# Performance work log

Measured on AMD Instinct MI355X. Metric: run time of the kernel, lower is better.

Reference implementation:

```python
import jax, jax.numpy as jnp
import numpy as np

B, H, S, DK, DV = 2, 16, 2048, 128, 128


def setup_inputs() -> dict:
    key = jax.random.key(0)
    kq, kk, kv = jax.random.split(key, 3)
    query = jax.random.normal(kq, (B, H, S, DK), dtype=jnp.float32)
    k_ = jax.random.normal(kk, (B, H, S, DK), dtype=jnp.float32)
    value = jax.random.normal(kv, (B, H, S, DV), dtype=jnp.float32)
    # causal mask: True = masked out (upper triangle above diagonal)
    causal = ~jnp.tril(jnp.ones((S, S), dtype=bool))
    mask = jnp.broadcast_to(causal[None, None, :, :], (B, 1, S, S))
    return {"query": query, "key": k_, "value": value, "mask": mask}


def reference(query, key, value, mask):
    d_k = query.shape[-1]
    # scores: (B, H, Sq, Sk)
    scores = jnp.einsum("bhqd,bhkd->bhqk", query, key) / jnp.sqrt(jnp.float32(d_k))
    scores = jnp.where(mask, -jnp.inf, scores)
    attention_weights = jax.nn.softmax(scores, axis=-1)
    # dropout p=0.0 (eval) -> identity
    output = jnp.einsum("bhqk,bhkv->bhqv", attention_weights, value)
    return (output, attention_weights)
```

## Files before the change

### kernel.cpp

```cpp
#include <hip/hip_runtime.h>
#include <hip/hip_bf16.h>


typedef __attribute__((ext_vector_type(4))) float  f32x4;
typedef __attribute__((ext_vector_type(8))) short  short8;
typedef __attribute__((ext_vector_type(4))) short  short4v;

#define S_LEN 2048
#define DKK   128
#define QBLK  128
#define KBLK  64
#define NBH   32
#define NW    8

__device__ __forceinline__ short f2bf(float f) {
    return __builtin_bit_cast(short, __float2bfloat16(f));
}

__device__ __forceinline__ void g2l16(const void* g, void* l) {
    __builtin_amdgcn_global_load_lds(
        (const __attribute__((address_space(1))) unsigned int*)g,
        (__attribute__((address_space(3))) unsigned int*)l, 16, 0, 0);
}


__global__ __launch_bounds__(256) void conv_kv(const float* __restrict__ K,
                                               const float* __restrict__ V,
                                               short* __restrict__ Kb,
                                               short* __restrict__ VT) {
    if (blockIdx.x < 2048) {
        const int NCH = NBH * S_LEN * (DKK / 8);
        for (int g = blockIdx.x * 256 + threadIdx.x; g < NCH; g += 2048 * 256) {
            const int row = g >> 4;
            const int c   = g & 15;
            const float* p = K + (size_t)row * DKK + c * 8;
            f32x4 a = *(const f32x4*)p;
            f32x4 b = *(const f32x4*)(p + 4);
            short8 r;
            #pragma unroll
            for (int j = 0; j < 4; ++j) {
                r[j]     = f2bf(a[j]);
                r[4 + j] = f2bf(b[j]);
            }
            *(short8*)(Kb + (size_t)row * DKK + (size_t)(c ^ (row & 7)) * 8) = r;
        }
    } else {
        __shared__ short tile[64][130];
        const int ib = blockIdx.x - 2048;
        const int bh = ib >> 5;
        const int kt = ib & 31;
        const float* Vb = V + ((size_t)bh * S_LEN + kt * 64) * DKK;
        const int t  = threadIdx.x;
        const int k8 = t >> 5, d0 = (t & 31) * 4;
        #pragma unroll
        for (int it = 0; it < 8; ++it) {
            int k = it * 8 + k8;
            f32x4 v = *(const f32x4*)(Vb + (size_t)k * DKK + d0);
            #pragma unroll
            for (int j = 0; j < 4; ++j) tile[k][d0 + j] = f2bf(v[j]);
        }
        __syncthreads();
        const int d = t >> 1, half = t & 1;
        short* outb = VT + (size_t)bh * DKK * S_LEN + (size_t)d * S_LEN + kt * 64;
        #pragma unroll
        for (int cc = 0; cc < 4; ++cc) {
            short8 r;
            #pragma unroll
            for (int j = 0; j < 8; ++j) r[j] = tile[half * 32 + cc * 8 + j][d];
            int cp = (half * 4 + cc) ^ (d & 7);
            *(short8*)(outb + cp * 8) = r;
        }
    }
}


__global__ __launch_bounds__(512) void attn_main(
    const float* __restrict__ Qf, const short* __restrict__ Kb,
    const short* __restrict__ VT, float* __restrict__ O,
    float* __restrict__ W)
{
    __shared__ __align__(16) short kT[2][KBLK * DKK];
    __shared__ __align__(16) short vtT[2][DKK * KBLK];
    __shared__ __align__(16) short pT[NW][16 * KBLK];

    const int tid  = threadIdx.x;
    const int lane = tid & 63;
    const int w    = tid >> 6;
    const int lg   = lane >> 4;
    const int lr   = lane & 15;
    const int s7   = lr & 7;

    const int i  = blockIdx.x;
    const int bh = (i & 7) * 4 + ((i >> 3) & 3);
    const int qt = 15 - (i >> 5);
    const int q0 = qt * QBLK;
    const int qbase = q0 + w * 16;
    const int kend  = q0 + QBLK;
    const int ntk   = kend / KBLK;
    const int ntk1  = qt + 1;
    const int qg    = qbase + lr;

    const short* Kbh = Kb + (size_t)bh * S_LEN * DKK;
    const short* VTb = VT + (size_t)bh * DKK * S_LEN;
    float* Ob = O + (size_t)bh * S_LEN * DKK;
    float* Wb = W + (size_t)bh * S_LEN * S_LEN;

    auto stage_k2 = [&](int buf, int kt2) {
        const char* gk = (const char*)(Kbh + (size_t)kt2 * 128 * DKK);
        char* lk = (char*)kT[buf];
        char* lv = (char*)vtT[buf];
        #pragma unroll
        for (int ii = 0; ii < 2; ++ii) {
            g2l16(gk + ii * 8192 + tid * 16,         lk + ii * 8192 + w * 1024);
            g2l16(gk + 16384 + ii * 8192 + tid * 16, lv + ii * 8192 + w * 1024);
        }
    };
    auto stage_k = [&](int buf, int kt_) {
        const char* gk = (const char*)(Kbh + (size_t)kt_ * KBLK * DKK);
        char* lk = (char*)kT[buf];
        #pragma unroll
        for (int ii = 0; ii < 2; ++ii)
            g2l16(gk + ii * 8192 + tid * 16, lk + ii * 8192 + w * 1024);
    };
    auto stage_v = [&](int buf, int kt_) {
        const char* gv = (const char*)VTb + (size_t)kt_ * (KBLK * 2);
        char* lv = (char*)vtT[buf];
        #pragma unroll
        for (int ii = 0; ii < 2; ++ii) {
            const int L = ii * 8192 + tid * 16;
            g2l16(gv + (size_t)(L >> 7) * (S_LEN * 2) + (L & 127),
                  lv + ii * 8192 + w * 1024);
        }
    };

    stage_k2(0, 0);
    if (ntk1 > 1) stage_k2(1, 1);

    const float QSCALE = 0.08838834764831845f * 1.4426950408889634f;
    short8 qf[4];
    {
        const float* qp = Qf + ((size_t)bh * S_LEN + qg) * DKK + lg * 8;
        #pragma unroll
        for (int ds = 0; ds < 4; ++ds) {
            f32x4 a = *(const f32x4*)(qp + ds * 32);
            f32x4 b = *(const f32x4*)(qp + ds * 32 + 4);
            short8 r;
            #pragma unroll
            for (int jj = 0; jj < 4; ++jj) {
                r[jj]     = f2bf(a[jj] * QSCALE);
                r[4 + jj] = f2bf(b[jj] * QSCALE);
            }
            qf[ds] = r;
        }
    }

    auto k_frag = [&](const char* kBc, int t, int ds) -> short8 {
        const int off = ((16 * t + lr) * 256 + ds * 64 + lg * 16) ^ (s7 << 4);
        return *(const short8*)(kBc + off);
    };

    float lsum = 0.f;
    int cur = 0;
    for (int kt_ = 0; kt_ < ntk1; ++kt_) {
        __syncthreads();
        if (kt_ >= 1 && kt_ + 1 < ntk1) stage_k2(cur ^ 1, kt_ + 1);
        const int k0 = kt_ * 128;
        const char* kLo = (const char*)kT[cur];
        const char* kHi = (const char*)vtT[cur];
        #pragma unroll
        for (int t = 0; t < 8; ++t) {
            const char* kBc = (t < 4) ? kLo : kHi;
            const int   tt  = t & 3;
            f32x4 d = {0.f, 0.f, 0.f, 0.f};
            __builtin_amdgcn_s_setprio(1);
            #pragma unroll
            for (int ds = 0; ds < 4; ++ds)
                d = __builtin_amdgcn_mfma_f32_16x16x32_bf16(
                        k_frag(kBc, tt, ds), qf[ds], d, 0, 0, 0);
            __builtin_amdgcn_s_setprio(0);
            const int kb = k0 + 16 * t + lg * 4;
            #pragma unroll
            for (int r = 0; r < 4; ++r)
                lsum += (kb + r <= qg) ? exp2f(d[r]) : 0.f;
        }
        cur ^= 1;
    }
    lsum += __shfl_xor(lsum, 16);
    lsum += __shfl_xor(lsum, 32);
    const float invl = 1.0f / lsum;

    f32x4 acc[8];
    #pragma unroll
    for (int ii = 0; ii < 8; ++ii) acc[ii] = (f32x4){0.f, 0.f, 0.f, 0.f};

    __syncthreads();
    cur = 0;
    stage_k(0, 0);
    stage_v(0, 0);
    for (int kt_ = 0; kt_ < ntk; ++kt_) {
        __syncthreads();
        if (kt_ + 1 < ntk) { stage_k(cur ^ 1, kt_ + 1); stage_v(cur ^ 1, kt_ + 1); }
        const int k0 = kt_ * KBLK;
        const char* kBc = (const char*)kT[cur];
        const char* vBc = (const char*)vtT[cur];
        char* pBc = (char*)pT[w];
        const bool live = (k0 <= qbase + 15);

        if (live) {
            #pragma unroll
            for (int t = 0; t < 4; ++t) {
                f32x4 d = {0.f, 0.f, 0.f, 0.f};
                __builtin_amdgcn_s_setprio(1);
                #pragma unroll
                for (int ds = 0; ds < 4; ++ds)
                    d = __builtin_amdgcn_mfma_f32_16x16x32_bf16(
                            k_frag(kBc, t, ds), qf[ds], d, 0, 0, 0);
                __builtin_amdgcn_s_setprio(0);
                const int kb = k0 + 16 * t + lg * 4;
                f32x4 pv;
                short4v pb;
                #pragma unroll
                for (int r = 0; r < 4; ++r) {
                    const float p = (kb + r <= qg) ? exp2f(d[r]) * invl : 0.f;
                    pv[r] = p;
                    pb[r] = f2bf(p);
                }
                *(f32x4*)(Wb + (size_t)qg * S_LEN + kb) = pv;
                const int poff = lr * 128 + (((16 * t + lg * 4) * 2) ^ (s7 << 4));
                *(short4v*)(pBc + poff) = pb;
            }
            #pragma unroll
            for (int h = 0; h < 2; ++h) {
                const int poff = lr * 128 + ((h * 64 + lg * 16) ^ (s7 << 4));
                short8 pa = *(const short8*)(pBc + poff);
                __builtin_amdgcn_s_setprio(1);
                #pragma unroll
                for (int nt = 0; nt < 8; ++nt) {
                    const int voff = (nt * 16 + lr) * 128 + ((h * 64 + lg * 16) ^ (s7 << 4));
                    short8 vf = *(const short8*)(vBc + voff);
                    acc[nt] = __builtin_amdgcn_mfma_f32_16x16x32_bf16(pa, vf, acc[nt], 0, 0, 0);
                }
                __builtin_amdgcn_s_setprio(0);
            }
        } else {
            const f32x4 z = {0.f, 0.f, 0.f, 0.f};
            #pragma unroll
            for (int t = 0; t < 4; ++t)
                *(f32x4*)(Wb + (size_t)qg * S_LEN + k0 + 16 * t + lg * 4) = z;
        }
        cur ^= 1;
    }

    #pragma unroll
    for (int nt = 0; nt < 8; ++nt)
        #pragma unroll
        for (int r = 0; r < 4; ++r)
            Ob[(size_t)(qbase + lg * 4 + r) * DKK + nt * 16 + lr] = acc[nt][r];

    const int zc = S_LEN - kend;
    if (zc > 0) {
        const int yo = tid >> 2;
        const int xo = tid & 3;
        float* wrow = Wb + (size_t)(q0 + yo) * S_LEN + kend;
        const f32x4 z = {0.f, 0.f, 0.f, 0.f};
        for (int c = xo * 4; c < zc; c += 16)
            *(f32x4*)(wrow + c) = z;
    }
}

extern "C" void kernel_launch(void* const* d_in, const int* in_sizes, int n_in,
                              void* d_out, int out_size, void* d_ws, size_t ws_size,
                              hipStream_t stream) {
    const float* Q = (const float*)d_in[0];
    const float* K = (const float*)d_in[1];
    const float* V = (const float*)d_in[2];
    float* O = (float*)d_out;
    float* W = (float*)d_out + (size_t)NBH * S_LEN * DKK;

    const size_t TEN = (size_t)NBH * S_LEN * DKK;
    short* Kb  = (short*)d_ws;
    short* VTw = Kb + TEN;

    conv_kv<<<3072, 256, 0, stream>>>(K, V, Kb, VTw);
    attn_main<<<NBH * (S_LEN / QBLK), 512, 0, stream>>>(Q, Kb, VTw, O, W);
}
```

Before: 211.3 us.

## Halve key block size to 32 and rework LDS swizzles and staging

Cuts the main-pass key/value tile from 64 to 32 keys and resizes the first (row-sum) pass to 64-key steps. V-transpose, P and K staging and their XOR swizzles are rewritten for 32-key rows, and the PV step becomes one MFMA k-slice per tile. The aim is finer causal skipping along the diagonal and smaller LDS staging per step, at the cost of twice as many barriers and loop iterations with less work per synchronization. LDS arrays keep their declared sizes, so less shared memory is actually used.

Result: slower. 231.7 us (+9.6%).

```diff
diff --git a/kernel.cpp b/kernel.cpp
--- a/kernel.cpp
+++ b/kernel.cpp
@@ -9,7 +9,7 @@
 #define S_LEN 2048
 #define DKK   128
 #define QBLK  128
-#define KBLK  64
+#define KBLK  32
 #define NBH   32
 #define NW    8
 
@@ -67,7 +67,7 @@
             short8 r;
             #pragma unroll
             for (int j = 0; j < 8; ++j) r[j] = tile[half * 32 + cc * 8 + j][d];
-            int cp = (half * 4 + cc) ^ (d & 7);
+            int cp = half * 4 + (cc ^ (d & 3));
             *(short8*)(outb + cp * 8) = r;
         }
     }
@@ -97,7 +97,7 @@
     const int qbase = q0 + w * 16;
     const int kend  = q0 + QBLK;
     const int ntk   = kend / KBLK;
-    const int ntk1  = qt + 1;
+    const int ntk1  = kend / 64;
     const int qg    = qbase + lr;
 
     const short* Kbh = Kb + (size_t)bh * S_LEN * DKK;
@@ -105,36 +105,26 @@
     float* Ob = O + (size_t)bh * S_LEN * DKK;
     float* Wb = W + (size_t)bh * S_LEN * S_LEN;
 
-    auto stage_k2 = [&](int buf, int kt2) {
-        const char* gk = (const char*)(Kbh + (size_t)kt2 * 128 * DKK);
+    auto stage_k64 = [&](int buf, int j64) {
+        const char* gk = (const char*)Kbh + (size_t)j64 * 16384;
         char* lk = (char*)kT[buf];
         char* lv = (char*)vtT[buf];
-        #pragma unroll
-        for (int ii = 0; ii < 2; ++ii) {
-            g2l16(gk + ii * 8192 + tid * 16,         lk + ii * 8192 + w * 1024);
-            g2l16(gk + 16384 + ii * 8192 + tid * 16, lv + ii * 8192 + w * 1024);
-        }
-    };
-    auto stage_k = [&](int buf, int kt_) {
-        const char* gk = (const char*)(Kbh + (size_t)kt_ * KBLK * DKK);
-        char* lk = (char*)kT[buf];
-        #pragma unroll
-        for (int ii = 0; ii < 2; ++ii)
-            g2l16(gk + ii * 8192 + tid * 16, lk + ii * 8192 + w * 1024);
-    };
-    auto stage_v = [&](int buf, int kt_) {
-        const char* gv = (const char*)VTb + (size_t)kt_ * (KBLK * 2);
-        char* lv = (char*)vtT[buf];
-        #pragma unroll
-        for (int ii = 0; ii < 2; ++ii) {
-            const int L = ii * 8192 + tid * 16;
-            g2l16(gv + (size_t)(L >> 7) * (S_LEN * 2) + (L & 127),
-                  lv + ii * 8192 + w * 1024);
-        }
-    };
-
-    stage_k2(0, 0);
-    if (ntk1 > 1) stage_k2(1, 1);
+        g2l16(gk + tid * 16,        lk + w * 1024);
+        g2l16(gk + 8192 + tid * 16, lv + w * 1024);
+    };
+    auto stage_k32 = [&](int buf, int j32) {
+        const char* gk = (const char*)Kbh + (size_t)j32 * 8192;
+        g2l16(gk + tid * 16, (char*)kT[buf] + w * 1024);
+    };
+    auto stage_v32 = [&](int buf, int j32) {
+        const char* gv = (const char*)VTb + (size_t)j32 * 64;
+        const int L = tid * 16;
+        g2l16(gv + (size_t)(L >> 6) * (S_LEN * 2) + (L & 63),
+              (char*)vtT[buf] + w * 1024);
+    };
+
+    stage_k64(0, 0);
+    if (ntk1 > 1) stage_k64(1, 1);
 
     const float QSCALE = 0.08838834764831845f * 1.4426950408889634f;
     short8 qf[4];
@@ -163,14 +153,14 @@
     int cur = 0;
     for (int kt_ = 0; kt_ < ntk1; ++kt_) {
         __syncthreads();
-        if (kt_ >= 1 && kt_ + 1 < ntk1) stage_k2(cur ^ 1, kt_ + 1);
-        const int k0 = kt_ * 128;
+        if (kt_ >= 1 && kt_ + 1 < ntk1) stage_k64(cur ^ 1, kt_ + 1);
+        const int k0 = kt_ * 64;
         const char* kLo = (const char*)kT[cur];
         const char* kHi = (const char*)vtT[cur];
         #pragma unroll
-        for (int t = 0; t < 8; ++t) {
-            const char* kBc = (t < 4) ? kLo : kHi;
-            const int   tt  = t & 3;
+        for (int t = 0; t < 4; ++t) {
+            const char* kBc = (t < 2) ? kLo : kHi;
+            const int   tt  = t & 1;
             f32x4 d = {0.f, 0.f, 0.f, 0.f};
             __builtin_amdgcn_s_setprio(1);
             #pragma unroll
@@ -195,11 +185,11 @@
 
     __syncthreads();
     cur = 0;
-    stage_k(0, 0);
-    stage_v(0, 0);
+    stage_k32(0, 0);
+    stage_v32(0, 0);
     for (int kt_ = 0; kt_ < ntk; ++kt_) {
         __syncthreads();
-        if (kt_ + 1 < ntk) { stage_k(cur ^ 1, kt_ + 1); stage_v(cur ^ 1, kt_ + 1); }
+        if (kt_ + 1 < ntk) { stage_k32(cur ^ 1, kt_ + 1); stage_v32(cur ^ 1, kt_ + 1); }
         const int k0 = kt_ * KBLK;
         const char* kBc = (const char*)kT[cur];
         const char* vBc = (const char*)vtT[cur];
@@ -208,7 +198,7 @@
 
         if (live) {
             #pragma unroll
-            for (int t = 0; t < 4; ++t) {
+            for (int t = 0; t < 2; ++t) {
                 f32x4 d = {0.f, 0.f, 0.f, 0.f};
                 __builtin_amdgcn_s_setprio(1);
                 #pragma unroll
@@ -226,26 +216,24 @@
                     pb[r] = f2bf(p);
                 }
                 *(f32x4*)(Wb + (size_t)qg * S_LEN + kb) = pv;
-                const int poff = lr * 128 + (((16 * t + lg * 4) * 2) ^ (s7 << 4));
+                const int poff = lr * 64 + ((((16 * t + lg * 4) * 2)) ^ ((lr & 3) << 4));
                 *(short4v*)(pBc + poff) = pb;
             }
-            #pragma unroll
-            for (int h = 0; h < 2; ++h) {
-                const int poff = lr * 128 + ((h * 64 + lg * 16) ^ (s7 << 4));
-                short8 pa = *(const short8*)(pBc + poff);
-                __builtin_amdgcn_s_setprio(1);
-                #pragma unroll
-                for (int nt = 0; nt < 8; ++nt) {
-                    const int voff = (nt * 16 + lr) * 128 + ((h * 64 + lg * 16) ^ (s7 << 4));
-                    short8 vf = *(const short8*)(vBc + voff);
-                    acc[nt] = __builtin_amdgcn_mfma_f32_16x16x32_bf16(pa, vf, acc[nt], 0, 0, 0);
-                }
-                __builtin_amdgcn_s_setprio(0);
-            }
+            const int poff = lr * 64 + ((lg * 16) ^ ((lr & 3) << 4));
+            short8 pa = *(const short8*)(pBc + poff);
+            __builtin_amdgcn_s_setprio(1);
+            #pragma unroll
+            for (int nt = 0; nt < 8; ++nt) {
+                const int dv   = nt * 16 + lr;
+                const int voff = dv * 64 + ((lg * 16) ^ ((dv & 3) << 4));
+                short8 vf = *(const short8*)(vBc + voff);
+                acc[nt] = __builtin_amdgcn_mfma_f32_16x16x32_bf16(pa, vf, acc[nt], 0, 0, 0);
+            }
+            __builtin_amdgcn_s_setprio(0);
         } else {
             const f32x4 z = {0.f, 0.f, 0.f, 0.f};
             #pragma unroll
-            for (int t = 0; t < 4; ++t)
+            for (int t = 0; t < 2; ++t)
                 *(f32x4*)(Wb + (size_t)qg * S_LEN + k0 + 16 * t + lg * 4) = z;
         }
         cur ^= 1;
```
